# Performance work log

Measured on AMD Instinct MI355X. Metric: run time of the kernel, lower is better.

The kernel has to match this reference:

```python
import jax, jax.numpy as jnp
import numpy as np

N_NODES = 100000
N_EDGES = 600000
N_GRAPHS = 512


def _glorot(key, shape):
    fan_in, fan_out = shape
    lim = np.sqrt(6.0 / (fan_in + fan_out)).astype(np.float32)
    return jax.random.uniform(key, shape, jnp.float32, -lim, lim)


def setup_inputs() -> dict:
    key = jax.random.key(0)
    ks = jax.random.split(key, 12)
    x = jax.random.normal(ks[0], (N_NODES, 3), jnp.float32)
    edge_index = jax.random.randint(ks[1], (2, N_EDGES), 0, N_NODES, jnp.int64)
    batch = jnp.sort(jax.random.randint(ks[2], (N_NODES,), 0, N_GRAPHS, jnp.int64))
    return {
        "x": x,
        "edge_index": edge_index,
        "batch": batch,
        "W1": _glorot(ks[3], (3, 128)),   "b1": jnp.zeros((128,), jnp.float32),
        "W2": _glorot(ks[4], (128, 128)), "b2": jnp.zeros((128,), jnp.float32),
        "W3": _glorot(ks[5], (128, 64)),  "b3": jnp.zeros((64,), jnp.float32),
        "Wl": _glorot(ks[6], (64, 1)),    "bl": jnp.zeros((1,), jnp.float32),
    }


def _gcn_conv(h, W, b, src, dst, deg_inv_sqrt):
    # linear transform, then normalized gather-scatter aggregation (self-loops
    # already included in src/dst and deg_inv_sqrt).
    h = h @ W                                            # [N, F_out]
    norm = deg_inv_sqrt[src] * deg_inv_sqrt[dst]         # [E+N]
    msg = h[src] * norm[:, None]                         # [E+N, F_out]
    out = jax.ops.segment_sum(msg, dst, num_segments=N_NODES)
    return out + b


def reference(x, edge_index, batch, W1, b1, W2, b2, W3, b3, Wl, bl):
    # add self-loops (GCNConv default add_self_loops=True)
    loop = jnp.arange(N_NODES, dtype=edge_index.dtype)
    src = jnp.concatenate([edge_index[0], loop])
    dst = jnp.concatenate([edge_index[1], loop])
    # symmetric normalization deg^{-1/2} (in-degree at target, edge weight 1)
    deg = jax.ops.segment_sum(jnp.ones_like(dst, jnp.float32), dst,
                              num_segments=N_NODES)
    deg_inv_sqrt = jnp.where(deg > 0, jax.lax.rsqrt(jnp.maximum(deg, 1.0)), 0.0)

    h = jax.nn.relu(_gcn_conv(x, W1, b1, src, dst, deg_inv_sqrt))
    h = jax.nn.relu(_gcn_conv(h, W2, b2, src, dst, deg_inv_sqrt))
    h = jax.nn.relu(_gcn_conv(h, W3, b3, src, dst, deg_inv_sqrt))

    # global mean pool over graphs
    sums = jax.ops.segment_sum(h, batch, num_segments=N_GRAPHS)    # [G, 64]
    counts = jax.ops.segment_sum(jnp.ones((N_NODES,), jnp.float32), batch,
                                 num_segments=N_GRAPHS)
    pooled = sums / jnp.maximum(counts, 1.0)[:, None]

    return pooled @ Wl + bl                                        # [G, 1]
```

## Files before the change

### kernel.cpp

```cpp
#include <hip/hip_runtime.h>

#define N_NODES 100000
#define N_EDGES 600000
#define N_GRAPHS 512
#define BSTRIDE 32

typedef __attribute__((ext_vector_type(8))) short short8;
typedef __attribute__((ext_vector_type(4))) float floatx4;
typedef __attribute__((ext_vector_type(2))) float floatx2;

__device__ __forceinline__ unsigned short f2bf(float f) {
    unsigned int u = __float_as_uint(f);
    u += 0x7FFFu + ((u >> 16) & 1u);
    return (unsigned short)(u >> 16);
}
__device__ __forceinline__ short8 pack8(const float* a) {
    short8 r;
    #pragma unroll
    for (int j = 0; j < 8; ++j) r[j] = (short)f2bf(a[j]);
    return r;
}

__device__ __forceinline__ uint2 pack_fp8x8(const float* v) {
    uint2 r;
    unsigned int a = 0;
    a = __builtin_amdgcn_cvt_pk_fp8_f32(v[0], v[1], a, 0);
    a = __builtin_amdgcn_cvt_pk_fp8_f32(v[2], v[3], a, 1);
    unsigned int b = 0;
    b = __builtin_amdgcn_cvt_pk_fp8_f32(v[4], v[5], b, 0);
    b = __builtin_amdgcn_cvt_pk_fp8_f32(v[6], v[7], b, 1);
    r.x = a; r.y = b;
    return r;
}
__device__ __forceinline__ unsigned char f2fp8(float v) {
    return (unsigned char)(__builtin_amdgcn_cvt_pk_fp8_f32(v, v, 0u, 0) & 0xFFu);
}
__device__ __forceinline__ void fma4_fp8(float* a, unsigned int w, float n) {
    floatx2 p;
    p = __builtin_amdgcn_cvt_pk_f32_fp8(w, 0); a[0] = fmaf(p[0], n, a[0]); a[1] = fmaf(p[1], n, a[1]);
    p = __builtin_amdgcn_cvt_pk_f32_fp8(w, 1); a[2] = fmaf(p[0], n, a[2]); a[3] = fmaf(p[1], n, a[3]);
}
__device__ __forceinline__ void init4_fp8(float* a, unsigned int w, float s) {
    floatx2 p;
    p = __builtin_amdgcn_cvt_pk_f32_fp8(w, 0); a[0] = p[0] * s; a[1] = p[1] * s;
    p = __builtin_amdgcn_cvt_pk_f32_fp8(w, 1); a[2] = p[0] * s; a[3] = p[1] * s;
}
__device__ __forceinline__ void fma16_fp8(float* a, uint4 v, float n) {
    fma4_fp8(a +  0, v.x, n); fma4_fp8(a +  4, v.y, n);
    fma4_fp8(a +  8, v.z, n); fma4_fp8(a + 12, v.w, n);
}
__device__ __forceinline__ void init16_fp8(float* a, uint4 v, float s) {
    init4_fp8(a +  0, v.x, s); init4_fp8(a +  4, v.y, s);
    init4_fp8(a +  8, v.z, s); init4_fp8(a + 12, v.w, s);
}

__device__ __forceinline__ void pack_one(const float* __restrict__ W, unsigned short* __restrict__ out,
                                         int idx, int N) {
    int lane = idx & 63;
    int ks = (idx >> 6) & 3;
    int ct = idx >> 8;
    int n = ct * 16 + (lane & 15);
    int kbase = ks * 32 + (lane >> 4) * 8;
    #pragma unroll
    for (int j = 0; j < 8; ++j)
        out[(size_t)idx * 8 + j] = f2bf(W[(size_t)(kbase + j) * N + n]);
}

#define NB_E ((N_EDGES + 255) / 256)
__global__ void k_build_pack(const int* __restrict__ src, const int* __restrict__ dst,
                             int* __restrict__ deg, int* __restrict__ bsrc,
                             const float* __restrict__ W2, const float* __restrict__ W3,
                             unsigned short* __restrict__ Wp2, unsigned short* __restrict__ Wp3) {
    if (blockIdx.x >= NB_E) {
        int idx = (blockIdx.x - NB_E) * 256 + threadIdx.x;
        if (idx < 2048) pack_one(W2, Wp2, idx, 128);
        else if (idx < 3072) pack_one(W3, Wp3, idx - 2048, 64);
        return;
    }
    int e = blockIdx.x * 256 + threadIdx.x;
    if (e >= N_EDGES) return;
    int d = dst[e];
    int slot = atomicAdd(&deg[d], 1);
    if (slot < BSTRIDE) bsrc[d * BSTRIDE + slot] = src[e];
}

#define NB1 6250
__global__ __launch_bounds__(256) void k_node1(const float* __restrict__ x,
                                               const int* __restrict__ deg,
                                               const int* __restrict__ bsrc,
                                               const float* __restrict__ W1,
                                               const float* __restrict__ b1,
                                               unsigned char* __restrict__ out) {
    int tid = threadIdx.x;
    __shared__ float Ws[384];
    __shared__ float bs[128];
    for (int i = tid; i < 384; i += 256) Ws[i] = W1[i];
    if (tid < 128) bs[tid] = b1[tid];
    __syncthreads();
    int gw = (blockIdx.x * 256 + tid) >> 6;
    int lane = tid & 63;
    int sub = lane >> 4, l16 = lane & 15;
    int node = gw * 4 + sub;
    int dgn = deg[node];
    float dnode = rsqrtf((float)(dgn + 1));
    int b0 = node * BSTRIDE;
    float p0 = 0.f, p1 = 0.f, p2 = 0.f;
    for (int u = l16; u < dgn; u += 16) {
        int s = bsrc[b0 + u];
        float n = rsqrtf((float)(deg[s] + 1)) * dnode;
        p0 = fmaf(x[s * 3 + 0], n, p0);
        p1 = fmaf(x[s * 3 + 1], n, p1);
        p2 = fmaf(x[s * 3 + 2], n, p2);
    }
    #pragma unroll
    for (int m = 8; m > 0; m >>= 1) {
        p0 += __shfl_xor(p0, m, 64);
        p1 += __shfl_xor(p1, m, 64);
        p2 += __shfl_xor(p2, m, 64);
    }
    float s2 = dnode * dnode;
    float a0 = fmaf(x[node * 3 + 0], s2, p0);
    float a1 = fmaf(x[node * 3 + 1], s2, p1);
    float a2 = fmaf(x[node * 3 + 2], s2, p2);
    int f = l16 * 8;
    float v[8];
    #pragma unroll
    for (int j = 0; j < 8; ++j)
        v[j] = fmaxf(bs[f + j] + a0 * Ws[f + j] + a1 * Ws[128 + f + j] + a2 * Ws[256 + f + j], 0.f);
    *(uint2*)(out + (size_t)node * 128 + f) = pack_fp8x8(v);
}

__global__ __launch_bounds__(256) void k_layer23(const unsigned char* __restrict__ h1,
                                                 const int* __restrict__ deg,
                                                 const int* __restrict__ bsrc,
                                                 const unsigned short* __restrict__ Wp2,
                                                 const float* __restrict__ b2,
                                                 const unsigned short* __restrict__ Wp3,
                                                 unsigned char* __restrict__ Q2f8) {
    __shared__ unsigned short Asb[32][136];
    __shared__ unsigned short Hsb[32][136];
    int tid = threadIdx.x;
    int wave = tid >> 6, lane = tid & 63;
    int quad = lane >> 4, m16 = lane & 15;
    int base = blockIdx.x * 32;

    {
        int sub = lane >> 3, l8 = lane & 7;
        int r = wave * 8 + sub;
        int node = base + r;
        int dgn = deg[node];
        float dnode = rsqrtf((float)(dgn + 1));
        int b0 = node * BSTRIDE;
        int idx[8]; float nn[8];
        #pragma unroll
        for (int u = 0; u < 8; ++u) {
            int s = bsrc[b0 + (u < dgn ? u : 0)];
            if ((unsigned)s >= N_NODES) s = node;
            idx[u] = s;
            nn[u] = (u < dgn) ? rsqrtf((float)(deg[s] + 1)) * dnode : 0.0f;
        }
        uint4 self = *(const uint4*)(h1 + (size_t)node * 128 + l8 * 16);
        uint4 g[8];
        #pragma unroll
        for (int u = 0; u < 8; ++u)
            g[u] = *(const uint4*)(h1 + (size_t)idx[u] * 128 + l8 * 16);
        float a[16];
        init16_fp8(a, self, dnode * dnode);
        #pragma unroll
        for (int u = 0; u < 8; ++u) fma16_fp8(a, g[u], nn[u]);
        for (int eb = 8; eb < dgn; eb += 8) {
            int idx2[8]; float nn2[8];
            #pragma unroll
            for (int u = 0; u < 8; ++u) {
                int uu = eb + u;
                int s = bsrc[b0 + (uu < dgn ? uu : 0)];
                if ((unsigned)s >= N_NODES) s = node;
                idx2[u] = s;
                nn2[u] = (uu < dgn) ? rsqrtf((float)(deg[s] + 1)) * dnode : 0.0f;
            }
            uint4 g2[8];
            #pragma unroll
            for (int u = 0; u < 8; ++u)
                g2[u] = *(const uint4*)(h1 + (size_t)idx2[u] * 128 + l8 * 16);
            #pragma unroll
            for (int u = 0; u < 8; ++u) fma16_fp8(a, g2[u], nn2[u]);
        }
        *(short8*)(&Asb[r][l8 * 16])     = pack8(a);
        *(short8*)(&Asb[r][l8 * 16 + 8]) = pack8(a + 8);
    }
    __syncthreads();

    int mt = wave & 1;
    int ch = wave >> 1;
    {
        short8 af[4];
        #pragma unroll
        for (int ks = 0; ks < 4; ++ks)
            af[ks] = *(const short8*)(&Asb[mt * 16 + m16][ks * 32 + quad * 8]);
        floatx4 acc[4];
        #pragma unroll
        for (int ct = 0; ct < 4; ++ct) acc[ct] = (floatx4){0.f, 0.f, 0.f, 0.f};
        #pragma unroll
        for (int ct = 0; ct < 4; ++ct) {
            int gct = ch * 4 + ct;
            #pragma unroll
            for (int ks = 0; ks < 4; ++ks) {
                short8 bf = *(const short8*)(Wp2 + ((size_t)(gct * 4 + ks) * 64 + lane) * 8);
                acc[ct] = __builtin_amdgcn_mfma_f32_16x16x32_bf16(af[ks], bf, acc[ct], 0, 0, 0);
            }
        }
        #pragma unroll
        for (int ct = 0; ct < 4; ++ct) {
            int col = (ch * 4 + ct) * 16 + m16;
            float bv = b2[col];
            #pragma unroll
            for (int r = 0; r < 4; ++r) {
                int row = mt * 16 + quad * 4 + r;
                Hsb[row][col] = f2bf(fmaxf(acc[ct][r] + bv, 0.0f));
            }
        }
    }
    __syncthreads();

    {
        int cp = wave >> 1;
        short8 hf[4];
        #pragma unroll
        for (int ks = 0; ks < 4; ++ks)
            hf[ks] = *(const short8*)(&Hsb[mt * 16 + m16][ks * 32 + quad * 8]);
        floatx4 acc3[2];
        acc3[0] = (floatx4){0.f, 0.f, 0.f, 0.f};
        acc3[1] = (floatx4){0.f, 0.f, 0.f, 0.f};
        #pragma unroll
        for (int ct = 0; ct < 2; ++ct) {
            int gct = cp * 2 + ct;
            #pragma unroll
            for (int ks = 0; ks < 4; ++ks) {
                short8 bf = *(const short8*)(Wp3 + ((size_t)(gct * 4 + ks) * 64 + lane) * 8);
                acc3[ct] = __builtin_amdgcn_mfma_f32_16x16x32_bf16(hf[ks], bf, acc3[ct], 0, 0, 0);
            }
        }
        #pragma unroll
        for (int ct = 0; ct < 2; ++ct) {
            int col = (cp * 2 + ct) * 16 + m16;
            #pragma unroll
            for (int r = 0; r < 4; ++r) {
                long row = base + mt * 16 + quad * 4 + r;
                Q2f8[row * 64 + col] = f2fp8(acc3[ct][r]);
            }
        }
    }
}

__global__ __launch_bounds__(256) void k_agg64_dot(const unsigned char* __restrict__ h,
                                                   const int* __restrict__ deg,
                                                   const int* __restrict__ bsrc,
                                                   const float* __restrict__ bias,
                                                   const float* __restrict__ Wl,
                                                   float* __restrict__ s_out) {
    int gw = (blockIdx.x * 256 + threadIdx.x) >> 6;
    if (gw >= N_NODES / 16) return;
    int lane = threadIdx.x & 63;
    int sub = lane >> 2, l4 = lane & 3;
    int node = gw * 16 + sub;
    int dgn = deg[node];
    float dnode = rsqrtf((float)(dgn + 1));
    int b0 = node * BSTRIDE;
    int idx[8]; float nn[8];
    #pragma unroll
    for (int u = 0; u < 8; ++u) {
        int s = bsrc[b0 + (u < dgn ? u : 0)];
        if ((unsigned)s >= N_NODES) s = node;
        idx[u] = s;
        nn[u] = (u < dgn) ? rsqrtf((float)(deg[s] + 1)) * dnode : 0.0f;
    }
    uint4 self = *(const uint4*)(h + (size_t)node * 64 + l4 * 16);
    uint4 g[8];
    #pragma unroll
    for (int u = 0; u < 8; ++u)
        g[u] = *(const uint4*)(h + (size_t)idx[u] * 64 + l4 * 16);
    float a[16];
    init16_fp8(a, self, dnode * dnode);
    #pragma unroll
    for (int u = 0; u < 8; ++u) fma16_fp8(a, g[u], nn[u]);
    for (int eb = 8; eb < dgn; eb += 8) {
        int idx2[8]; float nn2[8];
        #pragma unroll
        for (int u = 0; u < 8; ++u) {
            int uu = eb + u;
            int s = bsrc[b0 + (uu < dgn ? uu : 0)];
            if ((unsigned)s >= N_NODES) s = node;
            idx2[u] = s;
            nn2[u] = (uu < dgn) ? rsqrtf((float)(deg[s] + 1)) * dnode : 0.0f;
        }
        uint4 g2[8];
        #pragma unroll
        for (int u = 0; u < 8; ++u)
            g2[u] = *(const uint4*)(h + (size_t)idx2[u] * 64 + l4 * 16);
        #pragma unroll
        for (int u = 0; u < 8; ++u) fma16_fp8(a, g2[u], nn2[u]);
    }
    int f = l4 * 16;
    float v = 0.f;
    #pragma unroll
    for (int j = 0; j < 16; ++j)
        v = fmaf(fmaxf(a[j] + bias[f + j], 0.f), Wl[f + j], v);
    v += __shfl_xor(v, 1, 64);
    v += __shfl_xor(v, 2, 64);
    if (l4 == 0) s_out[node] = v;
}

__global__ __launch_bounds__(256) void k_pool2(const float* __restrict__ s,
                                               const int* __restrict__ batch,
                                               const float* __restrict__ bl,
                                               float* __restrict__ out) {
    int g = blockIdx.x;
    int tid = threadIdx.x;
    int lo = 0, hi = N_NODES;
    while (lo < hi) { int m = (lo + hi) >> 1; if (batch[m] < g) lo = m + 1; else hi = m; }
    int lo2 = lo, hi2 = N_NODES;
    while (lo2 < hi2) { int m = (lo2 + hi2) >> 1; if (batch[m] < g + 1) lo2 = m + 1; else hi2 = m; }
    float acc = 0.0f;
    for (int n = lo + tid; n < lo2; n += 256) acc += s[n];
    __shared__ float sm[256];
    sm[tid] = acc; __syncthreads();
    for (int off = 128; off > 0; off >>= 1) {
        if (tid < off) sm[tid] += sm[tid + off];
        __syncthreads();
    }
    if (tid == 0) out[g] = sm[0] / fmaxf((float)(lo2 - lo), 1.0f) + bl[0];
}

extern "C" void kernel_launch(void* const* d_in, const int* in_sizes, int n_in,
                              void* d_out, int out_size, void* d_ws, size_t ws_size,
                              hipStream_t stream) {
    const float* x     = (const float*)d_in[0];
    const int*   ei    = (const int*)d_in[1];
    const int*   batch = (const int*)d_in[2];
    const float* W1 = (const float*)d_in[3];
    const float* b1 = (const float*)d_in[4];
    const float* W2 = (const float*)d_in[5];
    const float* b2 = (const float*)d_in[6];
    const float* W3 = (const float*)d_in[7];
    const float* b3 = (const float*)d_in[8];
    const float* Wl = (const float*)d_in[9];
    const float* bl = (const float*)d_in[10];
    float* out = (float*)d_out;

    const int* e_src = ei;
    const int* e_dst = ei + N_EDGES;

    char* ws = (char*)d_ws;
    size_t off = 0;
    auto alloc = [&](size_t bytes) -> char* {
        char* p = ws + off;
        off = (off + bytes + 255) & ~(size_t)255;
        return p;
    };
    int*   deg   = (int*)  alloc((size_t)N_NODES * 4);
    int*   bsrc  = (int*)  alloc((size_t)N_NODES * BSTRIDE * 4);
    float* nscal = (float*)alloc((size_t)N_NODES * 4);
    unsigned char*  P1f8 = (unsigned char*) alloc((size_t)N_NODES * 128);
    unsigned char*  Q2f8 = (unsigned char*) alloc((size_t)N_NODES * 64);
    unsigned short* Wp2  = (unsigned short*)alloc((size_t)128 * 128 * 2);
    unsigned short* Wp3  = (unsigned short*)alloc((size_t)128 * 64 * 2);

    hipMemsetAsync(deg, 0, (size_t)N_NODES * 4, stream);

    k_build_pack<<<NB_E + 12, 256, 0, stream>>>(e_src, e_dst, deg, bsrc, W2, W3, Wp2, Wp3);

    k_node1<<<NB1, 256, 0, stream>>>(x, deg, bsrc, W1, b1, P1f8);

    k_layer23<<<N_NODES / 32, 256, 0, stream>>>(P1f8, deg, bsrc, Wp2, b2, Wp3, Q2f8);

    k_agg64_dot<<<(N_NODES / 16 + 3) / 4, 256, 0, stream>>>(Q2f8, deg, bsrc, b3, Wl, nscal);

    k_pool2<<<N_GRAPHS, 256, 0, stream>>>(nscal, batch, bl, out);
}
```

Measured before the change: 199.7 us.

## Pre-scale node features by deg^-1/2 to drop per-edge degree gathers

Folds the symmetric normalization into the stored features: each layer's output is multiplied by the node's deg^-1/2 before storing, and the aggregated sum is multiplied by the target's deg^-1/2 afterwards. The per-edge deg[s] gathers and rsqrt calls are removed. The first 8 neighbor indices are also loaded as two vector loads, and degree loops are clamped to BSTRIDE. This removes a dependent random gather per edge, at the cost of slightly different fp8 rounding because pre-scaled values are quantized.

```diff
diff --git a/kernel.cpp b/kernel.cpp
--- a/kernel.cpp
+++ b/kernel.cpp
@@ -14,10 +14,10 @@
     u += 0x7FFFu + ((u >> 16) & 1u);
     return (unsigned short)(u >> 16);
 }
-__device__ __forceinline__ short8 pack8(const float* a) {
+__device__ __forceinline__ short8 pack8s(const float* a, float s) {
     short8 r;
     #pragma unroll
-    for (int j = 0; j < 8; ++j) r[j] = (short)f2bf(a[j]);
+    for (int j = 0; j < 8; ++j) r[j] = (short)f2bf(a[j] * s);
     return r;
 }
 
@@ -40,18 +40,18 @@
     p = __builtin_amdgcn_cvt_pk_f32_fp8(w, 0); a[0] = fmaf(p[0], n, a[0]); a[1] = fmaf(p[1], n, a[1]);
     p = __builtin_amdgcn_cvt_pk_f32_fp8(w, 1); a[2] = fmaf(p[0], n, a[2]); a[3] = fmaf(p[1], n, a[3]);
 }
-__device__ __forceinline__ void init4_fp8(float* a, unsigned int w, float s) {
+__device__ __forceinline__ void init4_fp8(float* a, unsigned int w) {
     floatx2 p;
-    p = __builtin_amdgcn_cvt_pk_f32_fp8(w, 0); a[0] = p[0] * s; a[1] = p[1] * s;
-    p = __builtin_amdgcn_cvt_pk_f32_fp8(w, 1); a[2] = p[0] * s; a[3] = p[1] * s;
+    p = __builtin_amdgcn_cvt_pk_f32_fp8(w, 0); a[0] = p[0]; a[1] = p[1];
+    p = __builtin_amdgcn_cvt_pk_f32_fp8(w, 1); a[2] = p[0]; a[3] = p[1];
 }
 __device__ __forceinline__ void fma16_fp8(float* a, uint4 v, float n) {
     fma4_fp8(a +  0, v.x, n); fma4_fp8(a +  4, v.y, n);
     fma4_fp8(a +  8, v.z, n); fma4_fp8(a + 12, v.w, n);
 }
-__device__ __forceinline__ void init16_fp8(float* a, uint4 v, float s) {
-    init4_fp8(a +  0, v.x, s); init4_fp8(a +  4, v.y, s);
-    init4_fp8(a +  8, v.z, s); init4_fp8(a + 12, v.w, s);
+__device__ __forceinline__ void init16_fp8(float* a, uint4 v) {
+    init4_fp8(a +  0, v.x); init4_fp8(a +  4, v.y);
+    init4_fp8(a +  8, v.z); init4_fp8(a + 12, v.w);
 }
 
 __device__ __forceinline__ void pack_one(const float* __restrict__ W, unsigned short* __restrict__ out,
@@ -102,10 +102,11 @@
     int sub = lane >> 4, l16 = lane & 15;
     int node = gw * 4 + sub;
     int dgn = deg[node];
+    int dgb = dgn < BSTRIDE ? dgn : BSTRIDE;
     float dnode = rsqrtf((float)(dgn + 1));
     int b0 = node * BSTRIDE;
     float p0 = 0.f, p1 = 0.f, p2 = 0.f;
-    for (int u = l16; u < dgn; u += 16) {
+    for (int u = l16; u < dgb; u += 16) {
         int s = bsrc[b0 + u];
         float n = rsqrtf((float)(deg[s] + 1)) * dnode;
         p0 = fmaf(x[s * 3 + 0], n, p0);
@@ -126,7 +127,8 @@
     float v[8];
     #pragma unroll
     for (int j = 0; j < 8; ++j)
-        v[j] = fmaxf(bs[f + j] + a0 * Ws[f + j] + a1 * Ws[128 + f + j] + a2 * Ws[256 + f + j], 0.f);
+        v[j] = fmaxf(bs[f + j] + a0 * Ws[f + j] + a1 * Ws[128 + f + j] + a2 * Ws[256 + f + j], 0.f)
+               * dnode;
     *(uint2*)(out + (size_t)node * 128 + f) = pack_fp8x8(v);
 }
 
@@ -139,6 +141,7 @@
                                                  unsigned char* __restrict__ Q2f8) {
     __shared__ unsigned short Asb[32][136];
     __shared__ unsigned short Hsb[32][136];
+    __shared__ float disS[32];
     int tid = threadIdx.x;
     int wave = tid >> 6, lane = tid & 63;
     int quad = lane >> 4, m16 = lane & 15;
@@ -149,15 +152,20 @@
         int r = wave * 8 + sub;
         int node = base + r;
         int dgn = deg[node];
+        int dgb = dgn < BSTRIDE ? dgn : BSTRIDE;
         float dnode = rsqrtf((float)(dgn + 1));
-        int b0 = node * BSTRIDE;
-        int idx[8]; float nn[8];
+        if (l8 == 0) disS[r] = dnode;
+        const int* bp = bsrc + node * BSTRIDE;
+        uint4 i0 = *(const uint4*)(bp);
+        uint4 i1 = *(const uint4*)(bp + 4);
+        int idx[8] = {(int)i0.x, (int)i0.y, (int)i0.z, (int)i0.w,
+                      (int)i1.x, (int)i1.y, (int)i1.z, (int)i1.w};
+        float nn[8];
         #pragma unroll
         for (int u = 0; u < 8; ++u) {
-            int s = bsrc[b0 + (u < dgn ? u : 0)];
-            if ((unsigned)s >= N_NODES) s = node;
-            idx[u] = s;
-            nn[u] = (u < dgn) ? rsqrtf((float)(deg[s] + 1)) * dnode : 0.0f;
+            bool val = (u < dgb) && ((unsigned)idx[u] < N_NODES);
+            if (!val) idx[u] = node;
+            nn[u] = (u < dgb) ? 1.0f : 0.0f;
         }
         uint4 self = *(const uint4*)(h1 + (size_t)node * 128 + l8 * 16);
         uint4 g[8];
@@ -165,18 +173,18 @@
         for (int u = 0; u < 8; ++u)
             g[u] = *(const uint4*)(h1 + (size_t)idx[u] * 128 + l8 * 16);
         float a[16];
-        init16_fp8(a, self, dnode * dnode);
+        init16_fp8(a, self);
         #pragma unroll
         for (int u = 0; u < 8; ++u) fma16_fp8(a, g[u], nn[u]);
-        for (int eb = 8; eb < dgn; eb += 8) {
+        for (int eb = 8; eb < dgb; eb += 8) {
             int idx2[8]; float nn2[8];
             #pragma unroll
             for (int u = 0; u < 8; ++u) {
                 int uu = eb + u;
-                int s = bsrc[b0 + (uu < dgn ? uu : 0)];
+                int s = bsrc[bp - bsrc + (uu < dgb ? uu : 0)];
                 if ((unsigned)s >= N_NODES) s = node;
                 idx2[u] = s;
-                nn2[u] = (uu < dgn) ? rsqrtf((float)(deg[s] + 1)) * dnode : 0.0f;
+                nn2[u] = (uu < dgb) ? 1.0f : 0.0f;
             }
             uint4 g2[8];
             #pragma unroll
@@ -185,8 +193,8 @@
             #pragma unroll
             for (int u = 0; u < 8; ++u) fma16_fp8(a, g2[u], nn2[u]);
         }
-        *(short8*)(&Asb[r][l8 * 16])     = pack8(a);
-        *(short8*)(&Asb[r][l8 * 16 + 8]) = pack8(a + 8);
+        *(short8*)(&Asb[r][l8 * 16])     = pack8s(a, dnode);
+        *(short8*)(&Asb[r][l8 * 16 + 8]) = pack8s(a + 8, dnode);
     }
     __syncthreads();
 
@@ -245,8 +253,9 @@
             int col = (cp * 2 + ct) * 16 + m16;
             #pragma unroll
             for (int r = 0; r < 4; ++r) {
-                long row = base + mt * 16 + quad * 4 + r;
-                Q2f8[row * 64 + col] = f2fp8(acc3[ct][r]);
+                int rr = mt * 16 + quad * 4 + r;
+                long row = base + rr;
+                Q2f8[row * 64 + col] = f2fp8(acc3[ct][r] * disS[rr]);
             }
         }
     }
@@ -264,15 +273,19 @@
     int sub = lane >> 2, l4 = lane & 3;
     int node = gw * 16 + sub;
     int dgn = deg[node];
+    int dgb = dgn < BSTRIDE ? dgn : BSTRIDE;
     float dnode = rsqrtf((float)(dgn + 1));
-    int b0 = node * BSTRIDE;
-    int idx[8]; float nn[8];
+    const int* bp = bsrc + node * BSTRIDE;
+    uint4 i0 = *(const uint4*)(bp);
+    uint4 i1 = *(const uint4*)(bp + 4);
+    int idx[8] = {(int)i0.x, (int)i0.y, (int)i0.z, (int)i0.w,
+                  (int)i1.x, (int)i1.y, (int)i1.z, (int)i1.w};
+    float nn[8];
     #pragma unroll
     for (int u = 0; u < 8; ++u) {
-        int s = bsrc[b0 + (u < dgn ? u : 0)];
-        if ((unsigned)s >= N_NODES) s = node;
-        idx[u] = s;
-        nn[u] = (u < dgn) ? rsqrtf((float)(deg[s] + 1)) * dnode : 0.0f;
+        bool val = (u < dgb) && ((unsigned)idx[u] < N_NODES);
+        if (!val) idx[u] = node;
+        nn[u] = (u < dgb) ? 1.0f : 0.0f;
     }
     uint4 self = *(const uint4*)(h + (size_t)node * 64 + l4 * 16);
     uint4 g[8];
@@ -280,18 +293,18 @@
     for (int u = 0; u < 8; ++u)
         g[u] = *(const uint4*)(h + (size_t)idx[u] * 64 + l4 * 16);
     float a[16];
-    init16_fp8(a, self, dnode * dnode);
+    init16_fp8(a, self);
     #pragma unroll
     for (int u = 0; u < 8; ++u) fma16_fp8(a, g[u], nn[u]);
-    for (int eb = 8; eb < dgn; eb += 8) {
+    for (int eb = 8; eb < dgb; eb += 8) {
         int idx2[8]; float nn2[8];
         #pragma unroll
         for (int u = 0; u < 8; ++u) {
             int uu = eb + u;
-            int s = bsrc[b0 + (uu < dgn ? uu : 0)];
+            int s = bp[uu < dgb ? uu : 0];
             if ((unsigned)s >= N_NODES) s = node;
             idx2[u] = s;
-            nn2[u] = (uu < dgn) ? rsqrtf((float)(deg[s] + 1)) * dnode : 0.0f;
+            nn2[u] = (uu < dgb) ? 1.0f : 0.0f;
         }
         uint4 g2[8];
         #pragma unroll
@@ -304,7 +317,7 @@
     float v = 0.f;
     #pragma unroll
     for (int j = 0; j < 16; ++j)
-        v = fmaf(fmaxf(a[j] + bias[f + j], 0.f), Wl[f + j], v);
+        v = fmaf(fmaxf(fmaf(a[j], dnode, bias[f + j]), 0.f), Wl[f + j], v);
     v += __shfl_xor(v, 1, 64);
     v += __shfl_xor(v, 2, 64);
     if (l4 == 0) s_out[node] = v;
```

Result: faster. 176.1 us (-11.8%).
